# Kernel tuning notes

Measured on AMD Instinct MI355X. Metric: run time of the kernel, lower is better.

The kernel has to match this reference:

```python
import jax, jax.numpy as jnp
import numpy as np

N = 50000      # nodes
E = 800000     # edges (before self-loops)
F_IN = 256     # input features
HID = 32       # per-head hidden channels, conv1
H1 = 4         # heads conv1 (concat)
H2 = 4         # heads conv2 (mean)
NCLS = 40      # output classes
NEG_SLOPE = 0.2
SM_EPS = 1e-16  # PyG softmax denominator eps
LN_EPS = 1e-5


def setup_inputs() -> dict:
    key = jax.random.key(0)
    ks = jax.random.split(key, 12)
    s1 = 1.0 / np.sqrt(F_IN)
    s2 = 1.0 / np.sqrt(H1 * HID)
    return {
        "x": jax.random.normal(ks[0], (N, F_IN), dtype=jnp.float32),
        "edge_index": jax.random.randint(ks[1], (2, E), 0, N, dtype=jnp.int32),
        "W1": jax.random.normal(ks[2], (F_IN, H1 * HID), dtype=jnp.float32) * s1,
        "att_src1": jax.random.normal(ks[3], (H1, HID), dtype=jnp.float32) * s1,
        "att_dst1": jax.random.normal(ks[4], (H1, HID), dtype=jnp.float32) * s1,
        "b1": jnp.zeros((H1 * HID,), jnp.float32),
        "W2": jax.random.normal(ks[5], (H1 * HID, H2 * NCLS), dtype=jnp.float32) * s2,
        "att_src2": jax.random.normal(ks[6], (H2, NCLS), dtype=jnp.float32) * s2,
        "att_dst2": jax.random.normal(ks[7], (H2, NCLS), dtype=jnp.float32) * s2,
        "b2": jnp.zeros((NCLS,), jnp.float32),
        "ln0_g": jnp.ones((H1 * HID,), jnp.float32),
        "ln0_b": jnp.zeros((H1 * HID,), jnp.float32),
        "ln1_g": jnp.ones((NCLS,), jnp.float32),
        "ln1_b": jnp.zeros((NCLS,), jnp.float32),
    }


def gat_conv(x, edge_index, W, a_src, a_dst, bias, heads, ch, concat):
    """PyG GATConv: self-loops, edge attention, per-dst segment softmax, scatter-sum."""
    n = x.shape[0]
    loops = jnp.arange(n, dtype=edge_index.dtype)
    src = jnp.concatenate([edge_index[0], loops])  # message source
    dst = jnp.concatenate([edge_index[1], loops])  # aggregation target
    h = (x @ W).reshape(n, heads, ch)              # [N,H,C]
    e_src = jnp.einsum('nhc,hc->nh', h, a_src)     # [N,H]
    e_dst = jnp.einsum('nhc,hc->nh', h, a_dst)
    e = jax.nn.leaky_relu(e_src[src] + e_dst[dst], NEG_SLOPE)  # [E',H]
    m = jax.ops.segment_max(e, dst, num_segments=n)            # stable softmax max
    p = jnp.exp(e - m[dst])
    denom = jax.ops.segment_sum(p, dst, num_segments=n)
    alpha = p / (denom[dst] + SM_EPS)                          # [E',H]
    out = jax.ops.segment_sum(h[src] * alpha[:, :, None], dst, num_segments=n)  # [N,H,C]
    out = out.reshape(n, heads * ch) if concat else out.mean(axis=1)
    return out + bias


def layer_norm(x, g, b):
    mu = x.mean(axis=-1, keepdims=True)
    var = jnp.mean((x - mu) ** 2, axis=-1, keepdims=True)
    return (x - mu) * jax.lax.rsqrt(var + LN_EPS) * g + b


def reference(x, edge_index, W1, att_src1, att_dst1, b1, W2, att_src2, att_dst2, b2,
              ln0_g, ln0_b, ln1_g, ln1_b):
    # eval mode: dropout = identity
    h = gat_conv(x, edge_index, W1, att_src1, att_dst1, b1, H1, HID, True)
    h = layer_norm(jax.nn.elu(h), ln0_g, ln0_b)
    h = gat_conv(h, edge_index, W2, att_src2, att_dst2, b2, H2, NCLS, False)
    h = layer_norm(h, ln1_g, ln1_b)
    return jax.nn.log_softmax(h, axis=1)
```

## Files before the change

kernel.cpp:

```cpp
#include <hip/hip_runtime.h>
#include <hip/hip_bf16.h>
#include <hip/hip_fp16.h>

#define NNODES 50000
#define MPAD   50048
#define NEDGES 800000
#define ETOT   (NEDGES + NNODES)
#define FIN    256
#define HEADS  4
#define C1     32
#define D1     128
#define C2     40
#define D2     160

#define CB  ((ETOT + 255) / 256)
#define RB1 144
#define RB2 88
#define GB1 (MPAD / 64)

typedef unsigned short u16;
typedef short v8s __attribute__((ext_vector_type(8)));
typedef float v4f __attribute__((ext_vector_type(4)));

__device__ __forceinline__ float bf2f(unsigned u) {
    union { unsigned u; float f; } x; x.u = u << 16; return x.f;
}
__device__ __forceinline__ u16 f2bf(float f) {
    unsigned u = __float_as_uint(f);
    return (u16)((u + 0x7fff + ((u >> 16) & 1)) >> 16);
}
__device__ __forceinline__ unsigned pk_bf16(float a, float b) {
    unsigned ua = (__float_as_uint(a) + 0x8000u) >> 16;
    unsigned ub = (__float_as_uint(b) + 0x8000u) & 0xffff0000u;
    return ub | ua;
}
__device__ __forceinline__ float wave_sum(float v) {
    #pragma unroll
    for (int m = 32; m > 0; m >>= 1) v += __shfl_xor(v, m, 64);
    return v;
}
__device__ __forceinline__ void wave_sum2(float& a, float& b) {
    #pragma unroll
    for (int m = 32; m > 0; m >>= 1) {
        a += __shfl_xor(a, m, 64);
        b += __shfl_xor(b, m, 64);
    }
}
__device__ __forceinline__ float leaky(float x) { return fmaxf(x, 0.2f * x); }

__device__ __forceinline__ void repack_body(const float* __restrict__ W,
                                            const float* __restrict__ as,
                                            const float* __restrict__ ad,
                                            u16* __restrict__ Wf,
                                            int K, int N, int C, int total, int idx) {
    if (idx >= total) return;
    int KS = K >> 5, NT = N >> 4;
    int j = idx & 7, lane = (idx >> 3) & 63;
    int rest = idx >> 9;
    int ks = rest % KS, nt = rest / KS;
    int k = ks * 32 + (lane >> 4) * 8 + j;
    int n16 = lane & 15;
    float val = 0.f;
    if (nt < NT) {
        val = W[(size_t)k * N + nt * 16 + n16];
    } else if (n16 < 8) {
        int h = n16 & 3;
        const float* av = (n16 < 4) ? as : ad;
        float s = 0.f;
        for (int c = 0; c < C; c++) s += W[(size_t)k * N + h * C + c] * av[h * C + c];
        val = s;
    }
    Wf[idx] = f2bf(val);
}

template <bool AF32, int KK, int NT>
__device__ __forceinline__ void gemm_body(const void* __restrict__ Aptr,
                                          const u16* __restrict__ Wf,
                                          u16* __restrict__ Out,
                                          float* __restrict__ ssrc,
                                          float* __restrict__ sdst, int M, int bid) {
    const int KS = KK / 32;
    const int NCOL = NT * 16;
    int wid = threadIdx.x >> 6, lane = threadIdx.x & 63;
    int r0 = bid * 64 + wid * 16;
    int m = lane & 15, quad = lane >> 4;
    int row = r0 + m;
    bool rowok = row < M;

    v8s a[KS];
    if (AF32) {
        const float* ap = (const float*)Aptr + (size_t)(rowok ? row : 0) * KK + quad * 8;
        #pragma unroll
        for (int ks = 0; ks < KS; ks++) {
            if (rowok) {
                float4 fa = *(const float4*)(ap + ks * 32);
                float4 fb = *(const float4*)(ap + ks * 32 + 4);
                union { unsigned u[4]; v8s v; } c;
                c.u[0] = pk_bf16(fa.x, fa.y); c.u[1] = pk_bf16(fa.z, fa.w);
                c.u[2] = pk_bf16(fb.x, fb.y); c.u[3] = pk_bf16(fb.z, fb.w);
                a[ks] = c.v;
            } else {
                a[ks] = (v8s){0,0,0,0,0,0,0,0};
            }
        }
    } else {
        const u16* ap = (const u16*)Aptr + (size_t)(rowok ? row : 0) * KK + quad * 8;
        #pragma unroll
        for (int ks = 0; ks < KS; ks++)
            a[ks] = rowok ? *(const v8s*)(ap + ks * 32) : (v8s){0,0,0,0,0,0,0,0};
    }

    const v8s* bp0 = (const v8s*)Wf + lane;
    #pragma unroll 2
    for (int nt = 0; nt < NT; nt++) {
        v4f acc = {0.f, 0.f, 0.f, 0.f};
        const v8s* bp = bp0 + nt * KS * 64;
        #pragma unroll
        for (int ks = 0; ks < KS; ks++)
            acc = __builtin_amdgcn_mfma_f32_16x16x32_bf16(a[ks], bp[ks * 64], acc, 0, 0, 0);
        int col = nt * 16 + m;
        #pragma unroll
        for (int reg = 0; reg < 4; reg++) {
            int r = r0 + quad * 4 + reg;
            if (r < M) Out[(size_t)r * NCOL + col] = f2bf(acc[reg]);
        }
    }
    {
        v4f acc = {0.f, 0.f, 0.f, 0.f};
        const v8s* bp = bp0 + NT * KS * 64;
        #pragma unroll
        for (int ks = 0; ks < KS; ks++)
            acc = __builtin_amdgcn_mfma_f32_16x16x32_bf16(a[ks], bp[ks * 64], acc, 0, 0, 0);
        if (m < 8) {
            float* tgt = (m < 4) ? ssrc : sdst;
            int h = m & 3;
            #pragma unroll
            for (int reg = 0; reg < 4; reg++) {
                int r = r0 + quad * 4 + reg;
                if (r < M) tgt[r * 4 + h] = acc[reg];
            }
        }
    }
}

__global__ __launch_bounds__(256) void count_repack(const int* __restrict__ ei,
                                                    int* __restrict__ counts,
                                                    const float* __restrict__ W1,
                                                    const float* __restrict__ as1,
                                                    const float* __restrict__ ad1,
                                                    u16* __restrict__ Wf1,
                                                    const float* __restrict__ W2,
                                                    const float* __restrict__ as2,
                                                    const float* __restrict__ ad2,
                                                    u16* __restrict__ Wf2) {
    int b = blockIdx.x;
    if (b < CB) {
        int t = b * 256 + threadIdx.x;
        if (t >= ETOT) return;
        int d = (t < NEDGES) ? ei[NEDGES + t] : (t - NEDGES);
        atomicAdd(&counts[d], 1);
    } else if (b < CB + RB1) {
        repack_body(W1, as1, ad1, Wf1, FIN, D1, C1, 9 * 8 * 512, (b - CB) * 256 + threadIdx.x);
    } else {
        repack_body(W2, as2, ad2, Wf2, D1, D2, C2, 11 * 4 * 512, (b - CB - RB1) * 256 + threadIdx.x);
    }
}

__global__ __launch_bounds__(1024) void scan_k(const int* __restrict__ counts, int* __restrict__ rowptr) {
    __shared__ int wsum[16];
    __shared__ int srun;
    const int t = threadIdx.x;
    const int lane = t & 63, wid = t >> 6;
    if (t == 0) srun = 0;
    __syncthreads();
    for (int base = 0; base < NNODES; base += 4096) {
        int i4 = base + t * 4;
        int4 v = make_int4(0, 0, 0, 0);
        if (i4 < NNODES) v = *(const int4*)(counts + i4);
        int tsum = v.x + v.y + v.z + v.w;
        int x = tsum;
        #pragma unroll
        for (int off = 1; off < 64; off <<= 1) {
            int y = __shfl_up(x, off, 64);
            if (lane >= off) x += y;
        }
        if (lane == 63) wsum[wid] = x;
        __syncthreads();
        if (wid == 0) {
            int w = (lane < 16) ? wsum[lane] : 0;
            #pragma unroll
            for (int off = 1; off < 16; off <<= 1) {
                int y = __shfl_up(w, off, 64);
                if (lane >= off) w += y;
            }
            if (lane < 16) wsum[lane] = w;
        }
        __syncthreads();
        int wbase = (wid > 0) ? wsum[wid - 1] : 0;
        int run = srun;
        int pre = run + wbase + x - tsum;
        if (i4 < NNODES) {
            rowptr[i4]     = pre;
            rowptr[i4 + 1] = pre + v.x;
            rowptr[i4 + 2] = pre + v.x + v.y;
            rowptr[i4 + 3] = pre + v.x + v.y + v.z;
        }
        __syncthreads();
        if (t == 1023) srun = run + wsum[15];
        __syncthreads();
    }
    if (t == 0) rowptr[NNODES] = srun;
}

__global__ __launch_bounds__(256) void gemm1_fill(const float* __restrict__ x,
                                                  const u16* __restrict__ Wf1,
                                                  u16* __restrict__ BH1,
                                                  float* __restrict__ ssrc,
                                                  float* __restrict__ sdst,
                                                  const int* __restrict__ ei,
                                                  const int* __restrict__ rowptr,
                                                  int* __restrict__ cursor,
                                                  u16* __restrict__ esrc) {
    if (blockIdx.x < GB1) {
        gemm_body<true, FIN, 8>(x, Wf1, BH1, ssrc, sdst, NNODES, blockIdx.x);
    } else {
        int t = (blockIdx.x - GB1) * 256 + threadIdx.x;
        if (t >= ETOT) return;
        int s, d;
        if (t < NEDGES) { s = ei[t]; d = ei[NEDGES + t]; } else { s = t - NEDGES; d = s; }
        int pos = atomicAdd(&cursor[d], 1);
        esrc[rowptr[d] + pos] = (u16)s;
    }
}

template <int KK, int NT>
__global__ __launch_bounds__(256) void gemm_mfma(const u16* __restrict__ A,
                                                 const u16* __restrict__ Wf,
                                                 u16* __restrict__ Out,
                                                 float* __restrict__ ssrc,
                                                 float* __restrict__ sdst, int M) {
    gemm_body<false, KK, NT>(A, Wf, Out, ssrc, sdst, M, blockIdx.x);
}

#define PHASE_A32(SRC_ARR, P_ARR)                                                  \
    int nj = end - tb; if (nj > 32) nj = 32;                                       \
    bool on1 = jj < nj, on2 = jj + 16 < nj;                                        \
    int sE1 = on1 ? (int)esrc[tb + jj] : 0;                                        \
    int sE2 = on2 ? (int)esrc[tb + 16 + jj] : 0;                                   \
    if (hh == 0) { if (on1) SRC_ARR[wid][jj] = sE1;                                \
                   if (on2) SRC_ARR[wid][16 + jj] = sE2; }                         \
    float pa = on1 ? __expf(leaky(ssrc[sE1 * 4 + hh] + sdh)) : 0.f;                \
    float pb = on2 ? __expf(leaky(ssrc[sE2 * 4 + hh] + sdh)) : 0.f;                \
    float tsum = pa + pb;                                                          \
    tsum += __shfl_xor(tsum, 1, 64); tsum += __shfl_xor(tsum, 2, 64);              \
    tsum += __shfl_xor(tsum, 4, 64); tsum += __shfl_xor(tsum, 8, 64);              \
    den += tsum;                                                                   \
    if (on1) P_ARR[wid][hh][jj] = pa;                                              \
    if (on2) P_ARR[wid][hh][16 + jj] = pb;

__global__ __launch_bounds__(256) void gat_fused1(const int* __restrict__ rowptr,
                                                  const u16* __restrict__ esrc,
                                                  const float* __restrict__ ssrc,
                                                  const float* __restrict__ sdst,
                                                  const u16* __restrict__ BH,
                                                  const float* __restrict__ b1,
                                                  const float* __restrict__ g,
                                                  const float* __restrict__ be,
                                                  u16* __restrict__ BOb) {
    __shared__ int   s_src[4][32];
    __shared__ float s_p[4][4][32];
    __shared__ float s_den[4][4];
    int wid = threadIdx.x >> 6, lane = threadIdx.x & 63;
    int node = blockIdx.x * 4 + wid;
    int jj = lane & 15, hh = lane >> 4;
    int l8 = lane & 15, grp = lane >> 4;
    int head = l8 >> 2;
    float sdh = sdst[node * 4 + hh];
    int beg = rowptr[node], end = rowptr[node + 1];
    float den = 0.f;
    float acc[8];
    #pragma unroll
    for (int i = 0; i < 8; i++) acc[i] = 0.f;

    for (int tb = beg; tb < end; tb += 32) {
        PHASE_A32(s_src, s_p)
        #pragma unroll 8
        for (int j = grp; j < nj; j += 4) {
            int sj = s_src[wid][j];
            float al = s_p[wid][head][j];
            uint4 h = *(const uint4*)(BH + (size_t)sj * D1 + l8 * 8);
            acc[0] += al * bf2f(h.x & 0xffffu); acc[1] += al * bf2f(h.x >> 16);
            acc[2] += al * bf2f(h.y & 0xffffu); acc[3] += al * bf2f(h.y >> 16);
            acc[4] += al * bf2f(h.z & 0xffffu); acc[5] += al * bf2f(h.z >> 16);
            acc[6] += al * bf2f(h.w & 0xffffu); acc[7] += al * bf2f(h.w >> 16);
        }
    }
    if (jj == 0) s_den[wid][hh] = den;
    #pragma unroll
    for (int i = 0; i < 8; i++) {
        acc[i] += __shfl_xor(acc[i], 16, 64);
        acc[i] += __shfl_xor(acc[i], 32, 64);
    }
    float rden = 1.f / s_den[wid][head];
    float4 bA = *(const float4*)(b1 + l8 * 8), bB = *(const float4*)(b1 + l8 * 8 + 4);
    float v[8];
    v[0] = acc[0] * rden + bA.x; v[1] = acc[1] * rden + bA.y;
    v[2] = acc[2] * rden + bA.z; v[3] = acc[3] * rden + bA.w;
    v[4] = acc[4] * rden + bB.x; v[5] = acc[5] * rden + bB.y;
    v[6] = acc[6] * rden + bB.z; v[7] = acc[7] * rden + bB.w;
    float s8 = 0.f, q8 = 0.f;
    #pragma unroll
    for (int i = 0; i < 8; i++) {
        v[i] = v[i] > 0.f ? v[i] : __expf(v[i]) - 1.f;
        s8 += v[i]; q8 += v[i] * v[i];
    }
    wave_sum2(s8, q8);
    float mu = s8 * (1.f / 512.f);
    float var = q8 * (1.f / 512.f) - mu * mu;
    float rs = rsqrtf(var + 1e-5f);
    if (grp == 0) {
        float4 gA = *(const float4*)(g + l8 * 8),  gB = *(const float4*)(g + l8 * 8 + 4);
        float4 eA = *(const float4*)(be + l8 * 8), eB = *(const float4*)(be + l8 * 8 + 4);
        u16 o[8] = {f2bf((v[0] - mu) * rs * gA.x + eA.x), f2bf((v[1] - mu) * rs * gA.y + eA.y),
                    f2bf((v[2] - mu) * rs * gA.z + eA.z), f2bf((v[3] - mu) * rs * gA.w + eA.w),
                    f2bf((v[4] - mu) * rs * gB.x + eB.x), f2bf((v[5] - mu) * rs * gB.y + eB.y),
                    f2bf((v[6] - mu) * rs * gB.z + eB.z), f2bf((v[7] - mu) * rs * gB.w + eB.w)};
        *(uint4*)(BOb + (size_t)node * D1 + l8 * 8) = *(uint4*)o;
    }
}

__global__ __launch_bounds__(256) void gat_fused2(const int* __restrict__ rowptr,
                                                  const u16* __restrict__ esrc,
                                                  const float* __restrict__ ssrc,
                                                  const float* __restrict__ sdst,
                                                  const u16* __restrict__ BH,
                                                  const float* __restrict__ b2,
                                                  const float* __restrict__ g,
                                                  const float* __restrict__ be,
                                                  float* __restrict__ out) {
    __shared__ int   s_src[4][32];
    __shared__ float s_p[4][4][32];
    __shared__ float s_den[4][4];
    __shared__ float scr3[4][3][160];
    int wid = threadIdx.x >> 6, lane = threadIdx.x & 63;
    int node = blockIdx.x * 4 + wid;
    int jj = lane & 15, hh = lane >> 4;
    int grp = lane / 20;
    int glane = lane - grp * 20;
    int head = glane / 5;
    float sdh = sdst[node * 4 + hh];
    int beg = rowptr[node], end = rowptr[node + 1];
    float den = 0.f;
    float acc[8];
    #pragma unroll
    for (int i = 0; i < 8; i++) acc[i] = 0.f;

    for (int tb = beg; tb < end; tb += 32) {
        PHASE_A32(s_src, s_p)
        if (grp < 3) {
            #pragma unroll 4
            for (int j = grp; j < nj; j += 3) {
                int sj = s_src[wid][j];
                float al = s_p[wid][head][j];
                uint4 h = *(const uint4*)(BH + (size_t)sj * D2 + glane * 8);
                acc[0] += al * bf2f(h.x & 0xffffu); acc[1] += al * bf2f(h.x >> 16);
                acc[2] += al * bf2f(h.y & 0xffffu); acc[3] += al * bf2f(h.y >> 16);
                acc[4] += al * bf2f(h.z & 0xffffu); acc[5] += al * bf2f(h.z >> 16);
                acc[6] += al * bf2f(h.w & 0xffffu); acc[7] += al * bf2f(h.w >> 16);
            }
        }
    }
    if (jj == 0) s_den[wid][hh] = den;
    if (grp < 3) {
        float rden = 1.f / s_den[wid][head];
        float4 oA = {acc[0] * rden, acc[1] * rden, acc[2] * rden, acc[3] * rden};
        float4 oB = {acc[4] * rden, acc[5] * rden, acc[6] * rden, acc[7] * rden};
        *(float4*)&scr3[wid][grp][glane * 8]     = oA;
        *(float4*)&scr3[wid][grp][glane * 8 + 4] = oB;
    }
    bool act = lane < 40;
    int c = act ? lane : 0;
    float o = 0.f;
    if (act) {
        float s = 0.f;
        #pragma unroll
        for (int k = 0; k < 4; k++)
            #pragma unroll
            for (int gg = 0; gg < 3; gg++) s += scr3[wid][gg][c + 40 * k];
        o = 0.25f * s + b2[c];
    }
    float so = act ? o : 0.f, qo = so * o;
    wave_sum2(so, qo);
    float mu = so * (1.f / 40.f);
    float var = qo * (1.f / 40.f) - mu * mu;
    float rs = rsqrtf(var + 1e-5f);
    float y = act ? (o - mu) * rs * g[c] + be[c] : 0.f;
    float ex = act ? __expf(y) : 0.f;
    float lse = __logf(wave_sum(ex));
    if (act) out[(size_t)node * 40 + c] = y - lse;
}

extern "C" void kernel_launch(void* const* d_in, const int* in_sizes, int n_in,
                              void* d_out, int out_size, void* d_ws, size_t ws_size,
                              hipStream_t stream) {
    const float* x   = (const float*)d_in[0];
    const int*   ei  = (const int*)d_in[1];
    const float* W1  = (const float*)d_in[2];
    const float* as1 = (const float*)d_in[3];
    const float* ad1 = (const float*)d_in[4];
    const float* b1  = (const float*)d_in[5];
    const float* W2  = (const float*)d_in[6];
    const float* as2 = (const float*)d_in[7];
    const float* ad2 = (const float*)d_in[8];
    const float* b2  = (const float*)d_in[9];
    const float* g0  = (const float*)d_in[10];
    const float* be0 = (const float*)d_in[11];
    const float* g1  = (const float*)d_in[12];
    const float* be1 = (const float*)d_in[13];

    float* ws = (float*)d_ws;
    u16*   BH1    = (u16*)ws;
    u16*   BH2    = (u16*)(ws + 3200000);
    u16*   BOb    = (u16*)(ws + 7200000);
    float* ssrc   = ws + 10400000;
    float* sdst   = ws + 10600000;
    int*   rowptr = (int*)(ws + 10800000);
    u16*   esrc   = (u16*)(ws + 10850004);
    int*   counts = (int*)(ws + 11275004);
    int*   cursor = (int*)(ws + 11325004);
    u16*   Wf1    = (u16*)(ws + 11375004);
    u16*   Wf2    = (u16*)(ws + 11393436);

    const int nb4 = NNODES / 4;

    hipMemsetAsync(counts, 0, 2 * NNODES * sizeof(int), stream);
    count_repack<<<CB + RB1 + RB2, 256, 0, stream>>>(ei, counts, W1, as1, ad1, Wf1,
                                                     W2, as2, ad2, Wf2);
    scan_k<<<1, 1024, 0, stream>>>(counts, rowptr);
    gemm1_fill<<<GB1 + CB, 256, 0, stream>>>(x, Wf1, BH1, ssrc, sdst, ei, rowptr, cursor, esrc);
    gat_fused1<<<nb4, 256, 0, stream>>>(rowptr, esrc, ssrc, sdst, BH1, b1, g0, be0, BOb);
    gemm_mfma<D1, 10><<<GB1, 256, 0, stream>>>(BOb, Wf2, BH2, ssrc, sdst, NNODES);
    gat_fused2<<<nb4, 256, 0, stream>>>(rowptr, esrc, ssrc, sdst, BH2, b2, g1, be1, (float*)d_out);
}
```

Baseline: 309.2 us.

## Overlap GEMM1 with CSR build and record per-edge slot during counting

The memset is replaced by a zeroing branch in the repack kernel. The layer-1 GEMM is split so its blocks run alongside the edge-count kernel and alongside the single-block scan, which hides the serial scan and the atomic counting. The atomic return value is now saved as a per-edge position, so the fill pass no longer needs a second atomic cursor and becomes a plain scatter with nontemporal stores. This adds a 1.7MB position buffer and an extra kernel launch, and the scan block is smaller at 256 threads, so it runs longer.

```diff
diff --git a/kernel.cpp b/kernel.cpp
--- a/kernel.cpp
+++ b/kernel.cpp
@@ -13,10 +13,13 @@
 #define C2     40
 #define D2     160
 
-#define CB  ((ETOT + 255) / 256)
-#define RB1 144
-#define RB2 88
-#define GB1 (MPAD / 64)
+#define CB   ((ETOT + 255) / 256)
+#define RB1  144
+#define RB2  88
+#define ZB   49
+#define GB1  (MPAD / 64)
+#define GB1A 391
+#define GB1B (GB1 - GB1A)
 
 typedef unsigned short u16;
 typedef short v8s __attribute__((ext_vector_type(8)));
@@ -143,62 +146,88 @@
     }
 }
 
-__global__ __launch_bounds__(256) void count_repack(const int* __restrict__ ei,
+__global__ __launch_bounds__(256) void zero_repack(int* __restrict__ counts,
+                                                   const float* __restrict__ W1,
+                                                   const float* __restrict__ as1,
+                                                   const float* __restrict__ ad1,
+                                                   u16* __restrict__ Wf1,
+                                                   const float* __restrict__ W2,
+                                                   const float* __restrict__ as2,
+                                                   const float* __restrict__ ad2,
+                                                   u16* __restrict__ Wf2) {
+    int b = blockIdx.x;
+    if (b < ZB) {
+        int i4 = (b * 256 + threadIdx.x) * 4;
+        if (i4 < NNODES) *(int4*)(counts + i4) = make_int4(0, 0, 0, 0);
+    } else if (b < ZB + RB1) {
+        repack_body(W1, as1, ad1, Wf1, FIN, D1, C1, 9 * 8 * 512, (b - ZB) * 256 + threadIdx.x);
+    } else {
+        repack_body(W2, as2, ad2, Wf2, D1, D2, C2, 11 * 4 * 512, (b - ZB - RB1) * 256 + threadIdx.x);
+    }
+}
+
+__global__ __launch_bounds__(256) void count_gemm1a(const int* __restrict__ ei,
                                                     int* __restrict__ counts,
-                                                    const float* __restrict__ W1,
-                                                    const float* __restrict__ as1,
-                                                    const float* __restrict__ ad1,
-                                                    u16* __restrict__ Wf1,
-                                                    const float* __restrict__ W2,
-                                                    const float* __restrict__ as2,
-                                                    const float* __restrict__ ad2,
-                                                    u16* __restrict__ Wf2) {
+                                                    u16* __restrict__ pos,
+                                                    const float* __restrict__ x,
+                                                    const u16* __restrict__ Wf1,
+                                                    u16* __restrict__ BH1,
+                                                    float* __restrict__ ssrc,
+                                                    float* __restrict__ sdst) {
     int b = blockIdx.x;
     if (b < CB) {
         int t = b * 256 + threadIdx.x;
         if (t >= ETOT) return;
         int d = (t < NEDGES) ? ei[NEDGES + t] : (t - NEDGES);
-        atomicAdd(&counts[d], 1);
-    } else if (b < CB + RB1) {
-        repack_body(W1, as1, ad1, Wf1, FIN, D1, C1, 9 * 8 * 512, (b - CB) * 256 + threadIdx.x);
+        pos[t] = (u16)atomicAdd(&counts[d], 1);
     } else {
-        repack_body(W2, as2, ad2, Wf2, D1, D2, C2, 11 * 4 * 512, (b - CB - RB1) * 256 + threadIdx.x);
-    }
-}
-
-__global__ __launch_bounds__(1024) void scan_k(const int* __restrict__ counts, int* __restrict__ rowptr) {
-    __shared__ int wsum[16];
+        gemm_body<true, FIN, 8>(x, Wf1, BH1, ssrc, sdst, NNODES, b - CB);
+    }
+}
+
+__global__ __launch_bounds__(256) void scan_gemm1b(const int* __restrict__ counts,
+                                                   int* __restrict__ rowptr,
+                                                   const float* __restrict__ x,
+                                                   const u16* __restrict__ Wf1,
+                                                   u16* __restrict__ BH1,
+                                                   float* __restrict__ ssrc,
+                                                   float* __restrict__ sdst) {
+    if (blockIdx.x > 0) {
+        gemm_body<true, FIN, 8>(x, Wf1, BH1, ssrc, sdst, NNODES, GB1A + blockIdx.x - 1);
+        return;
+    }
+    __shared__ int wsum[4];
     __shared__ int srun;
     const int t = threadIdx.x;
     const int lane = t & 63, wid = t >> 6;
     if (t == 0) srun = 0;
     __syncthreads();
-    for (int base = 0; base < NNODES; base += 4096) {
+    for (int base = 0; base < NNODES; base += 1024) {
         int i4 = base + t * 4;
         int4 v = make_int4(0, 0, 0, 0);
         if (i4 < NNODES) v = *(const int4*)(counts + i4);
         int tsum = v.x + v.y + v.z + v.w;
-        int x = tsum;
+        int xp = tsum;
         #pragma unroll
         for (int off = 1; off < 64; off <<= 1) {
-            int y = __shfl_up(x, off, 64);
-            if (lane >= off) x += y;
-        }
-        if (lane == 63) wsum[wid] = x;
+            int y = __shfl_up(xp, off, 64);
+            if (lane >= off) xp += y;
+        }
+        if (lane == 63) wsum[wid] = xp;
         __syncthreads();
         if (wid == 0) {
-            int w = (lane < 16) ? wsum[lane] : 0;
+            int w = (lane < 4) ? wsum[lane] : 0;
             #pragma unroll
-            for (int off = 1; off < 16; off <<= 1) {
+            for (int off = 1; off < 4; off <<= 1) {
                 int y = __shfl_up(w, off, 64);
                 if (lane >= off) w += y;
             }
-            if (lane < 16) wsum[lane] = w;
+            if (lane < 4) wsum[lane] = w;
         }
         __syncthreads();
         int wbase = (wid > 0) ? wsum[wid - 1] : 0;
         int run = srun;
-        int pre = run + wbase + x - tsum;
+        int pre = run + wbase + xp - tsum;
         if (i4 < NNODES) {
             rowptr[i4]     = pre;
             rowptr[i4 + 1] = pre + v.x;
@@ -206,31 +235,22 @@
             rowptr[i4 + 3] = pre + v.x + v.y + v.z;
         }
         __syncthreads();
-        if (t == 1023) srun = run + wsum[15];
+        if (t == 255) srun = run + wsum[3];
         __syncthreads();
     }
     if (t == 0) rowptr[NNODES] = srun;
 }
 
-__global__ __launch_bounds__(256) void gemm1_fill(const float* __restrict__ x,
-                                                  const u16* __restrict__ Wf1,
-                                                  u16* __restrict__ BH1,
-                                                  float* __restrict__ ssrc,
-                                                  float* __restrict__ sdst,
-                                                  const int* __restrict__ ei,
-                                                  const int* __restrict__ rowptr,
-                                                  int* __restrict__ cursor,
-                                                  u16* __restrict__ esrc) {
-    if (blockIdx.x < GB1) {
-        gemm_body<true, FIN, 8>(x, Wf1, BH1, ssrc, sdst, NNODES, blockIdx.x);
-    } else {
-        int t = (blockIdx.x - GB1) * 256 + threadIdx.x;
-        if (t >= ETOT) return;
-        int s, d;
-        if (t < NEDGES) { s = ei[t]; d = ei[NEDGES + t]; } else { s = t - NEDGES; d = s; }
-        int pos = atomicAdd(&cursor[d], 1);
-        esrc[rowptr[d] + pos] = (u16)s;
-    }
+__global__ __launch_bounds__(256) void fill_k(const int* __restrict__ ei,
+                                              const int* __restrict__ rowptr,
+                                              const u16* __restrict__ pos,
+                                              u16* __restrict__ esrc) {
+    int t = blockIdx.x * blockDim.x + threadIdx.x;
+    if (t >= ETOT) return;
+    int s, d;
+    if (t < NEDGES) { s = ei[t]; d = ei[NEDGES + t]; } else { s = t - NEDGES; d = s; }
+    int idx = rowptr[d] + (int)pos[t];
+    __builtin_nontemporal_store((u16)s, &esrc[idx]);
 }
 
 template <int KK, int NT>
@@ -427,17 +447,17 @@
     int*   rowptr = (int*)(ws + 10800000);
     u16*   esrc   = (u16*)(ws + 10850004);
     int*   counts = (int*)(ws + 11275004);
-    int*   cursor = (int*)(ws + 11325004);
-    u16*   Wf1    = (u16*)(ws + 11375004);
-    u16*   Wf2    = (u16*)(ws + 11393436);
+    u16*   pos    = (u16*)(ws + 11325004);
+    u16*   Wf1    = (u16*)(ws + 11750004);
+    u16*   Wf2    = (u16*)(ws + 11768436);
 
     const int nb4 = NNODES / 4;
 
-    hipMemsetAsync(counts, 0, 2 * NNODES * sizeof(int), stream);
-    count_repack<<<CB + RB1 + RB2, 256, 0, stream>>>(ei, counts, W1, as1, ad1, Wf1,
-                                                     W2, as2, ad2, Wf2);
-    scan_k<<<1, 1024, 0, stream>>>(counts, rowptr);
-    gemm1_fill<<<GB1 + CB, 256, 0, stream>>>(x, Wf1, BH1, ssrc, sdst, ei, rowptr, cursor, esrc);
+    zero_repack<<<ZB + RB1 + RB2, 256, 0, stream>>>(counts, W1, as1, ad1, Wf1,
+                                                    W2, as2, ad2, Wf2);
+    count_gemm1a<<<CB + GB1A, 256, 0, stream>>>(ei, counts, pos, x, Wf1, BH1, ssrc, sdst);
+    scan_gemm1b<<<1 + GB1B, 256, 0, stream>>>(counts, rowptr, x, Wf1, BH1, ssrc, sdst);
+    fill_k<<<CB, 256, 0, stream>>>(ei, rowptr, pos, esrc);
     gat_fused1<<<nb4, 256, 0, stream>>>(rowptr, esrc, ssrc, sdst, BH1, b1, g0, be0, BOb);
     gemm_mfma<D1, 10><<<GB1, 256, 0, stream>>>(BOb, Wf2, BH2, ssrc, sdst, NNODES);
     gat_fused2<<<nb4, 256, 0, stream>>>(rowptr, esrc, ssrc, sdst, BH2, b2, g1, be1, (float*)d_out);
```

After: 331.6 us. +7.2%, slower.
